# Kernel optimization log

Measured on AMD Instinct MI355X. Metric: run time of the kernel, lower is better.

## Reference

```python
import jax, jax.numpy as jnp
import numpy as np

B, T, V, K = 8, 256, 16, 8
L_SRL, L_VN = 66, 40  # PropBank / VerbNet label inventory sizes


def setup_inputs() -> dict:
    key = jax.random.key(0)
    ks = jax.random.split(key, 7)
    log_srl = jax.random.normal(ks[0], (B, T, T, L_SRL), jnp.float32)
    log_vn = jax.random.normal(ks[1], (B, T, T, L_VN), jnp.float32)
    v_label = jax.random.randint(ks[2], (B, V), 0, T)          # predicate token positions
    v_l = jax.random.randint(ks[3], (B,), 1, V + 1)            # num predicates per example
    orig_l = jax.random.randint(ks[4], (B,), T // 2, T + 1)    # original seq lengths
    semlink = jax.random.randint(ks[5], (B, V, 2, K), 0, L_VN) # [.,.,0,:]=srl label ids, [.,.,1,:]=vn label ids
    semlink_l = jax.random.randint(ks[6], (B, V), 0, K + 1)    # num semlink constraints per predicate
    return {"log_srl": log_srl, "log_vn": log_vn, "v_label": v_label,
            "v_l": v_l, "orig_l": orig_l, "semlink": semlink, "semlink_l": semlink_l}


def reference(log_srl, log_vn, v_label, v_l, orig_l, semlink, semlink_l):
    # log_srl: [B,T,T,L_srl], log_vn: [B,T,T,L_vn]
    Bn, Tn = log_srl.shape[0], log_srl.shape[1]
    Vn, Kn = v_label.shape[1], semlink.shape[-1]
    b = jnp.arange(Bn)[:, None]
    # Gather predicate rows: [B,V,T,L]
    sel_srl = log_srl[b, v_label]
    sel_vn = log_vn[b, v_label]
    # batch_index1_select: gather along label axis with semlink label ids -> [B,V,T,K]
    r_idx = semlink[:, :, 0, :]  # [B,V,K]
    a_idx = semlink[:, :, 1, :]
    g_r = jnp.take_along_axis(sel_srl, r_idx[:, :, None, :], axis=3)
    g_a = jnp.take_along_axis(sel_vn, a_idx[:, :, None, :], axis=3)
    diff = jnp.abs(g_r - g_a)  # [B,V,T,K]
    # masks: semlink length (len_to_mask), valid predicates, valid tokens (:orig_l)
    k_mask = jnp.arange(Kn)[None, None, :] < semlink_l[:, :, None]   # [B,V,K]
    v_mask = jnp.arange(Vn)[None, :] < v_l[:, None]                  # [B,V]
    t_mask = jnp.arange(Tn)[None, :] < orig_l[:, None]               # [B,T]
    mask = (k_mask[:, :, None, :] & v_mask[:, :, None, None] & t_mask[:, None, :, None])
    loss = jnp.sum(jnp.where(mask, diff, 0.0))
    num_prop = jnp.sum(v_l).astype(log_srl.dtype)  # use_gold_predicate == 1 normalizer
    return loss / num_prop
```

## Files before the change

kernel.cpp:

```cpp
#include <hip/hip_runtime.h>

#define Bn   8
#define Tn   256
#define Vn   16
#define Kn   8
#define LSRL 66
#define LVN  40

#define NBLK      128
#define SUM_SCALE 268435456.0
#define CNT_SHIFT 52
#define SUM_MASK  ((1ULL << CNT_SHIFT) - 1)
#define CNT_ONE   (1ULL << CNT_SHIFT)
#define POISON    0xAAAAAAAAAAAAAAAAULL
#define POISON_END_CNT (((POISON >> CNT_SHIFT) + NBLK) & 4095ULL)

__global__ __launch_bounds__(1024)
void semlink_onepass_kernel(const float* __restrict__ log_srl,
                            const float* __restrict__ log_vn,
                            const int*   __restrict__ v_label,
                            const int*   __restrict__ v_l,
                            const int*   __restrict__ orig_l,
                            const int*   __restrict__ semlink,
                            const int*   __restrict__ semlink_l,
                            unsigned long long* __restrict__ acc,
                            float*       __restrict__ out) {
    const int bv = blockIdx.x;
    const int b  = bv >> 4;
    const int v  = bv & 15;
    const int tid  = threadIdx.x;
    const int lane = tid & 63;
    const int wid  = tid >> 6;
    const int kq   = wid >> 2;
    const int tq   = wid & 3;
    const int t    = tq * 64 + lane;
    const int kbase = kq * 2;

    const int label = v_label[bv];
    const int sl    = semlink_l[bv];
    const int vl    = v_l[b];
    const int ol    = orig_l[b];
    const int* sl_base = semlink + bv * (2 * Kn);
    const int r0 = sl_base[kbase];
    const int r1 = sl_base[kbase + 1];
    const int a0 = sl_base[Kn + kbase];
    const int a1 = sl_base[Kn + kbase + 1];

    float local = 0.0f;
    if (v < vl && t < ol) {
        const size_t row = ((size_t)b * Tn + label) * Tn + t;
        const float* srl_row = log_srl + row * LSRL;
        const float* vn_row  = log_vn  + row * LVN;
        if (kbase     < sl) local += fabsf(srl_row[r0] - vn_row[a0]);
        if (kbase + 1 < sl) local += fabsf(srl_row[r1] - vn_row[a1]);
    }

    #pragma unroll
    for (int off = 32; off > 0; off >>= 1) local += __shfl_down(local, off);

    __shared__ float wsum[16];
    if (lane == 0) wsum[wid] = local;
    __syncthreads();

    if (tid == 0) {
        float bsum = 0.0f;
        #pragma unroll
        for (int w = 0; w < 16; ++w) bsum += wsum[w];

        unsigned long long pack =
            CNT_ONE + (unsigned long long)((double)bsum * SUM_SCALE + 0.5);
        unsigned long long old =
            __hip_atomic_fetch_add(acc, pack, __ATOMIC_ACQ_REL,
                                   __HIP_MEMORY_SCOPE_AGENT);

        int np = 0;
        #pragma unroll
        for (int bb = 0; bb < Bn; ++bb) np += v_l[bb];

        if ((old >> CNT_SHIFT) == (unsigned long long)(NBLK - 1)) {
            unsigned long long total =
                ((old & SUM_MASK) + (pack & SUM_MASK)) & SUM_MASK;
            out[0] = (float)((double)total / SUM_SCALE / (double)np);
            __hip_atomic_store(acc, 0ULL, __ATOMIC_RELEASE,
                               __HIP_MEMORY_SCOPE_AGENT);
        } else if (old == POISON) {
            unsigned long long cur;
            do {
                cur = __hip_atomic_load(acc, __ATOMIC_ACQUIRE,
                                        __HIP_MEMORY_SCOPE_AGENT);
            } while ((cur >> CNT_SHIFT) != POISON_END_CNT);
            unsigned long long total = (cur - POISON) & SUM_MASK;
            out[0] = (float)((double)total / SUM_SCALE / (double)np);
            __hip_atomic_store(acc, 0ULL, __ATOMIC_RELEASE,
                               __HIP_MEMORY_SCOPE_AGENT);
        }
    }
}

extern "C" void kernel_launch(void* const* d_in, const int* in_sizes, int n_in,
                              void* d_out, int out_size, void* d_ws, size_t ws_size,
                              hipStream_t stream) {
    const float* log_srl   = (const float*)d_in[0];
    const float* log_vn    = (const float*)d_in[1];
    const int*   v_label   = (const int*)d_in[2];
    const int*   v_l       = (const int*)d_in[3];
    const int*   orig_l    = (const int*)d_in[4];
    const int*   semlink   = (const int*)d_in[5];
    const int*   semlink_l = (const int*)d_in[6];
    float* out = (float*)d_out;
    unsigned long long* acc = (unsigned long long*)d_ws;

    semlink_onepass_kernel<<<NBLK, 1024, 0, stream>>>(
        log_srl, log_vn, v_label, v_l, orig_l, semlink, semlink_l, acc, out);
}
```

Baseline: 10.67 us.

## Split global atomic accumulator into four lines with two-level final reduction

Replaces the single global 64-bit atomic counter with four separate accumulator lines, each 128 bytes apart, so blocks hit four addresses instead of one. The last arriver on each line forwards that line's total into a final accumulator, and the last of those writes the output. It also relaxes the memory ordering from acq_rel/acquire to relaxed to avoid fence costs. This cuts same-address atomic contention at the price of an extra atomic hop on the critical path, and it relies on relaxed ordering being adequate for the packed-count scheme.

```diff
diff --git a/kernel.cpp b/kernel.cpp
--- a/kernel.cpp
+++ b/kernel.cpp
@@ -8,12 +8,18 @@
 #define LVN  40
 
 #define NBLK      128
+#define NLINE     4
+#define BPL       (NBLK / NLINE)
+#define LINE_STRIDE 16
+#define FINAL_IDX  56
+
 #define SUM_SCALE 268435456.0
 #define CNT_SHIFT 52
 #define SUM_MASK  ((1ULL << CNT_SHIFT) - 1)
 #define CNT_ONE   (1ULL << CNT_SHIFT)
 #define POISON    0xAAAAAAAAAAAAAAAAULL
-#define POISON_END_CNT (((POISON >> CNT_SHIFT) + NBLK) & 4095ULL)
+#define LINE_END_CNT  (((POISON >> CNT_SHIFT) + BPL)   & 4095ULL)
+#define FINAL_END_CNT (((POISON >> CNT_SHIFT) + NLINE) & 4095ULL)
 
 __global__ __launch_bounds__(1024)
 void semlink_onepass_kernel(const float* __restrict__ log_srl,
@@ -69,30 +75,59 @@
 
         unsigned long long pack =
             CNT_ONE + (unsigned long long)((double)bsum * SUM_SCALE + 0.5);
+
+        unsigned long long* line = acc + (bv & (NLINE - 1)) * LINE_STRIDE;
         unsigned long long old =
-            __hip_atomic_fetch_add(acc, pack, __ATOMIC_ACQ_REL,
+            __hip_atomic_fetch_add(line, pack, __ATOMIC_RELAXED,
                                    __HIP_MEMORY_SCOPE_AGENT);
 
-        int np = 0;
-        #pragma unroll
-        for (int bb = 0; bb < Bn; ++bb) np += v_l[bb];
-
-        if ((old >> CNT_SHIFT) == (unsigned long long)(NBLK - 1)) {
-            unsigned long long total =
-                ((old & SUM_MASK) + (pack & SUM_MASK)) & SUM_MASK;
-            out[0] = (float)((double)total / SUM_SCALE / (double)np);
-            __hip_atomic_store(acc, 0ULL, __ATOMIC_RELEASE,
-                               __HIP_MEMORY_SCOPE_AGENT);
+        unsigned long long line_total = 0;
+        bool forward = false;
+        if ((old >> CNT_SHIFT) == (unsigned long long)(BPL - 1)) {
+            line_total = (old + pack) & SUM_MASK;
+            forward = true;
         } else if (old == POISON) {
             unsigned long long cur;
             do {
-                cur = __hip_atomic_load(acc, __ATOMIC_ACQUIRE,
+                cur = __hip_atomic_load(line, __ATOMIC_RELAXED,
                                         __HIP_MEMORY_SCOPE_AGENT);
-            } while ((cur >> CNT_SHIFT) != POISON_END_CNT);
-            unsigned long long total = (cur - POISON) & SUM_MASK;
-            out[0] = (float)((double)total / SUM_SCALE / (double)np);
-            __hip_atomic_store(acc, 0ULL, __ATOMIC_RELEASE,
+            } while ((cur >> CNT_SHIFT) != LINE_END_CNT);
+            line_total = (cur - POISON) & SUM_MASK;
+            forward = true;
+        }
+
+        if (forward) {
+            __hip_atomic_store(line, 0ULL, __ATOMIC_RELAXED,
                                __HIP_MEMORY_SCOPE_AGENT);
+            unsigned long long* fin = acc + FINAL_IDX;
+            unsigned long long pack2 = CNT_ONE + line_total;
+            unsigned long long old2 =
+                __hip_atomic_fetch_add(fin, pack2, __ATOMIC_RELAXED,
+                                       __HIP_MEMORY_SCOPE_AGENT);
+
+            unsigned long long grand = 0;
+            bool finalize = false;
+            if ((old2 >> CNT_SHIFT) == (unsigned long long)(NLINE - 1)) {
+                grand = (old2 + pack2) & SUM_MASK;
+                finalize = true;
+            } else if (old2 == POISON) {
+                unsigned long long cur2;
+                do {
+                    cur2 = __hip_atomic_load(fin, __ATOMIC_RELAXED,
+                                             __HIP_MEMORY_SCOPE_AGENT);
+                } while ((cur2 >> CNT_SHIFT) != FINAL_END_CNT);
+                grand = (cur2 - POISON) & SUM_MASK;
+                finalize = true;
+            }
+
+            if (finalize) {
+                int np = 0;
+                #pragma unroll
+                for (int bb = 0; bb < Bn; ++bb) np += v_l[bb];
+                out[0] = (float)((double)grand / SUM_SCALE / (double)np);
+                __hip_atomic_store(fin, 0ULL, __ATOMIC_RELAXED,
+                                   __HIP_MEMORY_SCOPE_AGENT);
+            }
         }
     }
 }
```

After: 10.23 us, median of 2. 4.1% less time.
